# Kernel optimization log

Measured on AMD Instinct MI355X. Metric: run time of the kernel, lower is better.

## Reference

```python
import jax, jax.numpy as jnp
import numpy as np
import math

HIDDEN = 2048
NUM_HEADS = 32
NUM_KV_HEADS = 8
HEAD_DIM = HIDDEN // NUM_HEADS
GROUPS = NUM_HEADS // NUM_KV_HEADS
B, S = 2, 2048


def setup_inputs() -> dict:
    key = jax.random.key(0)
    ks = jax.random.split(key, 9)
    sc = 1.0 / math.sqrt(HIDDEN)
    x = jax.random.normal(ks[0], (B, S, HIDDEN), dtype=jnp.float32)
    # causal mask: 1 where attention allowed, 0 where masked
    mask = jnp.tril(jnp.ones((S, S), dtype=jnp.int32))[None, None, :, :]
    Wq = jax.random.normal(ks[1], (HIDDEN, HIDDEN), dtype=jnp.float32) * sc
    bq = jnp.zeros((HIDDEN,), dtype=jnp.float32)
    Wk = jax.random.normal(ks[2], (NUM_KV_HEADS * HEAD_DIM, HIDDEN), dtype=jnp.float32) * sc
    bk = jnp.zeros((NUM_KV_HEADS * HEAD_DIM,), dtype=jnp.float32)
    Wv = jax.random.normal(ks[3], (NUM_KV_HEADS * HEAD_DIM, HIDDEN), dtype=jnp.float32) * sc
    bv = jnp.zeros((NUM_KV_HEADS * HEAD_DIM,), dtype=jnp.float32)
    Wo = jax.random.normal(ks[4], (HIDDEN, HIDDEN), dtype=jnp.float32) * sc
    bo = jnp.zeros((HIDDEN,), dtype=jnp.float32)
    return {"x": x, "mask": mask, "Wq": Wq, "bq": bq, "Wk": Wk, "bk": bk,
            "Wv": Wv, "bv": bv, "Wo": Wo, "bo": bo}


def reference(x, mask, Wq, bq, Wk, bk, Wv, bv, Wo, bo):
    b, s, _ = x.shape
    # projections (torch Linear: y = x @ W.T + b)
    Q = (x @ Wq.T + bq).reshape(b, s, NUM_HEADS, HEAD_DIM).transpose(0, 2, 1, 3)  # b h s d
    K = (x @ Wk.T + bk).reshape(b, s, NUM_KV_HEADS, HEAD_DIM).transpose(0, 2, 1, 3)
    V = (x @ Wv.T + bv).reshape(b, s, NUM_KV_HEADS, HEAD_DIM).transpose(0, 2, 1, 3)
    # repeat_kv expansion
    K = jnp.repeat(K, GROUPS, axis=1)  # b h s d
    V = jnp.repeat(V, GROUPS, axis=1)
    scores = jnp.einsum('bhqd,bhkd->bhqk', Q, K) / math.sqrt(HEAD_DIM)
    scores = jnp.where(mask == 0, jnp.float32(-jnp.inf), scores)
    w = jax.nn.softmax(scores, axis=-1)
    # dropout is identity in eval mode
    out = jnp.einsum('bhqk,bhkd->bhqd', w, V)
    out = out.transpose(0, 2, 1, 3).reshape(b, s, HIDDEN)
    return out @ Wo.T + bo
```

## Files before the change

kernel.cpp:

```cpp
#include <hip/hip_runtime.h>
#include <hip/hip_bf16.h>
#include <stdint.h>

#define HID   2048
#define SLEN  2048
#define NB    2
#define NHEADS 32
#define NKVH   8
#define HDIM   64
#define KVW    512

typedef __bf16 bf16_t;
typedef __bf16 bf16x2 __attribute__((ext_vector_type(2)));
typedef __bf16 bf16x4 __attribute__((ext_vector_type(4)));
typedef __bf16 bf16x8 __attribute__((ext_vector_type(8)));
typedef float  f32x4  __attribute__((ext_vector_type(4)));

__device__ __forceinline__ f32x4 mfma16(bf16x8 a, bf16x8 b, f32x4 c) {
  return __builtin_amdgcn_mfma_f32_16x16x32_bf16(a, b, c, 0, 0, 0);
}

__device__ __forceinline__ void gl2lds16(const bf16_t* g, bf16_t* l) {
  __builtin_amdgcn_global_load_lds(
      (const __attribute__((address_space(1))) void*)g,
      (__attribute__((address_space(3))) void*)l,
      16, 0, 0);
}

__device__ __forceinline__ float fast_exp2(float x) {
#if __has_builtin(__builtin_amdgcn_exp2f)
  return __builtin_amdgcn_exp2f(x);
#else
  return __expf(x * 0.69314718f);
#endif
}

__device__ __forceinline__ bf16x8 ld8(const bf16_t* p) {
  return *(const bf16x8*)p;
}
__device__ __forceinline__ bf16x8 ld8(const float* p) {
  f32x4 a = *(const f32x4*)p;
  f32x4 b = *(const f32x4*)(p + 4);
  bf16x8 r;
  r[0] = (bf16_t)a[0]; r[1] = (bf16_t)a[1]; r[2] = (bf16_t)a[2]; r[3] = (bf16_t)a[3];
  r[4] = (bf16_t)b[0]; r[5] = (bf16_t)b[1]; r[6] = (bf16_t)b[2]; r[7] = (bf16_t)b[3];
  return r;
}

__device__ __forceinline__ uint32_t pack2(float a, float b) {
  bf16x2 t; t[0] = (bf16_t)a; t[1] = (bf16_t)b;
  return __builtin_bit_cast(uint32_t, t);
}

__device__ __forceinline__ void st_c(bf16_t* p, float v) { *p = (bf16_t)v; }
__device__ __forceinline__ void st_c(float*  p, float v) { *p = v; }

__global__ __launch_bounds__(256) void cvt_kernel(
    const float* __restrict__ x,  const float* __restrict__ wq,
    const float* __restrict__ wk, const float* __restrict__ wv,
    const float* __restrict__ wo,
    const float* __restrict__ bq, const float* __restrict__ bk,
    const float* __restrict__ bv,
    bf16_t* xb, bf16_t* wqb, bf16_t* wkb, bf16_t* wvb, bf16_t* wob,
    float* bcat)
{
  if (blockIdx.y >= 5) {
    const float* fs; float* fd; size_t n;
    if (blockIdx.y == 5)      { fs = bq; fd = bcat;        n = HID; }
    else if (blockIdx.y == 6) { fs = bk; fd = bcat + HID;  n = KVW; }
    else                      { fs = bv; fd = bcat + HID + KVW; n = KVW; }
    const size_t stride4 = (size_t)gridDim.x * 256 * 4;
    for (size_t i = ((size_t)blockIdx.x * 256 + threadIdx.x) * 4; i < n; i += stride4)
      *(f32x4*)(fd + i) = *(const f32x4*)(fs + i);
    return;
  }
  const float* s; bf16_t* d; size_t n;
  switch (blockIdx.y) {
    case 0:  s = x;  d = xb;  n = (size_t)NB * SLEN * HID; break;
    case 1:  s = wq; d = wqb; n = (size_t)HID * HID; break;
    case 2:  s = wk; d = wkb; n = (size_t)KVW * HID; break;
    case 3:  s = wv; d = wvb; n = (size_t)KVW * HID; break;
    default: s = wo; d = wob; n = (size_t)HID * HID; break;
  }
  const size_t stride = (size_t)gridDim.x * 256 * 8;
  for (size_t i = ((size_t)blockIdx.x * 256 + threadIdx.x) * 8; i < n; i += stride)
    *(bf16x8*)(d + i) = ld8(s + i);
}

__device__ __forceinline__ bf16x8 ldfrag(const bf16_t* __restrict__ Lh, int r, int g) {
  return *(const bf16x8*)(Lh + r * 64 + ((g ^ (r & 7)) << 3));
}

template <int Q>
__device__ __forceinline__ void mfma_quad(const bf16x8 (&af)[2][2],
                                          const bf16x8 (&bfr)[4][2],
                                          f32x4 (&acc)[8][4]) {
#pragma unroll
  for (int ks = 0; ks < 2; ++ks)
#pragma unroll
    for (int i = 0; i < 2; ++i)
#pragma unroll
      for (int ni = 0; ni < 4; ++ni)
        acc[2 * Q + i][ni] = mfma16(af[i][ks], bfr[ni][ks], acc[2 * Q + i][ni]);
}

__device__ __forceinline__ void phase_barrier() {
  __builtin_amdgcn_s_barrier();
  asm volatile("" ::: "memory");
}

__device__ __forceinline__ void gemm256_core(
    const bf16_t* __restrict__ Ag,
    const bf16_t* __restrict__ Bg,
    bf16_t* __restrict__ lds, f32x4 (&acc)[8][4])
{
  const int tid  = threadIdx.x;
  const int lane = tid & 63;
  const int w    = tid >> 6;
  const int fr   = lane & 15;
  const int quad = lane >> 4;
  const int wr   = w >> 2;
  const int wc   = w & 3;
  const int rbB  = (wc & 1) * 64;

  bf16_t* A0 = lds;
  bf16_t* B0 = lds + 16384;
  bf16_t* A1 = lds + 32768;
  bf16_t* B1 = lds + 49152;
  const bf16_t* Ar0 = A0 + wr * 8192;
  const bf16_t* Br0 = B0 + (wc >> 1) * 8192;
  const bf16_t* Ar1 = A1 + wr * 8192;
  const bf16_t* Br1 = B1 + (wc >> 1) * 8192;

  const f32x4 z4 = {0.f, 0.f, 0.f, 0.f};
#pragma unroll
  for (int i = 0; i < 8; ++i)
#pragma unroll
    for (int j = 0; j < 4; ++j) acc[i][j] = z4;

  auto STAGE = [&](const bf16_t* __restrict__ Gp, bf16_t* __restrict__ Lh) {
#pragma unroll
    for (int j = 0; j < 2; ++j) {
      const int s = j * 512 + tid;
      const int r = s >> 3;
      const int g = (s & 7) ^ (r & 7);
      gl2lds16(Gp + (size_t)r * HID + g * 8, Lh + s * 8);
    }
  };

  STAGE(Bg,                  B0);
  STAGE(Bg + 128 * HID,      B0 + 8192);
  STAGE(Ag,                  A0);
  STAGE(Ag + 128 * HID,      A0 + 8192);
  STAGE(Bg + 64,             B1);
  STAGE(Bg + 128 * HID + 64, B1 + 8192);
  asm volatile("s_waitcnt vmcnt(4)" ::: "memory");
  phase_barrier();

  bf16x8 bfr[4][2], af[2][2];

#pragma unroll 1
  for (int it = 0; it < 16; ++it) {
    const bool more = (it < 15);
    const size_t k1 = (size_t)(2 * it + 1) * 64;
    const size_t k2 = (size_t)(2 * it + 2) * 64;
    const size_t k3 = (size_t)(2 * it + 3) * 64;

#pragma unroll
    for (int ni = 0; ni < 4; ++ni)
#pragma unroll
      for (int ks = 0; ks < 2; ++ks)
        bfr[ni][ks] = ldfrag(Br0, rbB + ni * 16 + fr, ks * 4 + quad);
#pragma unroll
    for (int i = 0; i < 2; ++i)
#pragma unroll
      for (int ks = 0; ks < 2; ++ks)
        af[i][ks] = ldfrag(Ar0, i * 16 + fr, ks * 4 + quad);
    STAGE(Ag + k1, A1);
    phase_barrier();
    asm volatile("s_waitcnt lgkmcnt(0)" ::: "memory");
    __builtin_amdgcn_s_setprio(1);
    mfma_quad<0>(af, bfr, acc);
    __builtin_amdgcn_s_setprio(0);
    phase_barrier();

#pragma unroll
    for (int i = 0; i < 2; ++i)
#pragma unroll
      for (int ks = 0; ks < 2; ++ks)
        af[i][ks] = ldfrag(Ar0, 32 + i * 16 + fr, ks * 4 + quad);
    STAGE(Ag + 128 * HID + k1, A1 + 8192);
    phase_barrier();
    asm volatile("s_waitcnt lgkmcnt(0)" ::: "memory");
    __builtin_amdgcn_s_setprio(1);
    mfma_quad<1>(af, bfr, acc);
    __builtin_amdgcn_s_setprio(0);
    phase_barrier();

#pragma unroll
    for (int i = 0; i < 2; ++i)
#pragma unroll
      for (int ks = 0; ks < 2; ++ks)
        af[i][ks] = ldfrag(Ar0, 64 + i * 16 + fr, ks * 4 + quad);
    if (more) STAGE(Bg + k2, B0);
    phase_barrier();
    asm volatile("s_waitcnt lgkmcnt(0)" ::: "memory");
    __builtin_amdgcn_s_setprio(1);
    mfma_quad<2>(af, bfr, acc);
    __builtin_amdgcn_s_setprio(0);
    phase_barrier();

#pragma unroll
    for (int i = 0; i < 2; ++i)
#pragma unroll
      for (int ks = 0; ks < 2; ++ks)
        af[i][ks] = ldfrag(Ar0, 96 + i * 16 + fr, ks * 4 + quad);
    if (more) STAGE(Bg + 128 * HID + k2, B0 + 8192);
    phase_barrier();
    asm volatile("s_waitcnt lgkmcnt(0)" ::: "memory");
    __builtin_amdgcn_s_setprio(1);
    mfma_quad<3>(af, bfr, acc);
    __builtin_amdgcn_s_setprio(0);
    if (more) { asm volatile("s_waitcnt vmcnt(4)" ::: "memory"); }
    else      { asm volatile("s_waitcnt vmcnt(0)" ::: "memory"); }
    phase_barrier();

#pragma unroll
    for (int ni = 0; ni < 4; ++ni)
#pragma unroll
      for (int ks = 0; ks < 2; ++ks)
        bfr[ni][ks] = ldfrag(Br1, rbB + ni * 16 + fr, ks * 4 + quad);
#pragma unroll
    for (int i = 0; i < 2; ++i)
#pragma unroll
      for (int ks = 0; ks < 2; ++ks)
        af[i][ks] = ldfrag(Ar1, i * 16 + fr, ks * 4 + quad);
    if (more) STAGE(Ag + k2, A0);
    phase_barrier();
    asm volatile("s_waitcnt lgkmcnt(0)" ::: "memory");
    __builtin_amdgcn_s_setprio(1);
    mfma_quad<0>(af, bfr, acc);
    __builtin_amdgcn_s_setprio(0);
    phase_barrier();

#pragma unroll
    for (int i = 0; i < 2; ++i)
#pragma unroll
      for (int ks = 0; ks < 2; ++ks)
        af[i][ks] = ldfrag(Ar1, 32 + i * 16 + fr, ks * 4 + quad);
    if (more) STAGE(Ag + 128 * HID + k2, A0 + 8192);
    phase_barrier();
    asm volatile("s_waitcnt lgkmcnt(0)" ::: "memory");
    __builtin_amdgcn_s_setprio(1);
    mfma_quad<1>(af, bfr, acc);
    __builtin_amdgcn_s_setprio(0);
    phase_barrier();

#pragma unroll
    for (int i = 0; i < 2; ++i)
#pragma unroll
      for (int ks = 0; ks < 2; ++ks)
        af[i][ks] = ldfrag(Ar1, 64 + i * 16 + fr, ks * 4 + quad);
    if (more) STAGE(Bg + k3, B1);
    phase_barrier();
    asm volatile("s_waitcnt lgkmcnt(0)" ::: "memory");
    __builtin_amdgcn_s_setprio(1);
    mfma_quad<2>(af, bfr, acc);
    __builtin_amdgcn_s_setprio(0);
    phase_barrier();

#pragma unroll
    for (int i = 0; i < 2; ++i)
#pragma unroll
      for (int ks = 0; ks < 2; ++ks)
        af[i][ks] = ldfrag(Ar1, 96 + i * 16 + fr, ks * 4 + quad);
    if (more) STAGE(Bg + 128 * HID + k3, B1 + 8192);
    phase_barrier();
    asm volatile("s_waitcnt lgkmcnt(0)" ::: "memory");
    __builtin_amdgcn_s_setprio(1);
    mfma_quad<3>(af, bfr, acc);
    __builtin_amdgcn_s_setprio(0);
    if (more) { asm volatile("s_waitcnt vmcnt(4)" ::: "memory"); }
    phase_barrier();
  }
}

__global__ __launch_bounds__(512, 2) void qkv8_kernel(
    const bf16_t* __restrict__ xb, const bf16_t* __restrict__ Wcat,
    const float* __restrict__ bcat,
    bf16_t* __restrict__ Qb, bf16_t* __restrict__ Kb, bf16_t* __restrict__ VbT)
{
  __shared__ __align__(16) bf16_t lds[65536];
  const int cb = blockIdx.x;
  const int mb = blockIdx.y;
  f32x4 acc[8][4];
  gemm256_core(xb + (size_t)mb * 256 * HID, Wcat + (size_t)cb * 256 * HID, lds, acc);

  const int tid = threadIdx.x, lane = tid & 63, w = tid >> 6;
  const int fr = lane & 15, quad = lane >> 4, wr = w >> 2, wc = w & 3;
#pragma unroll
  for (int ni = 0; ni < 4; ++ni) {
    const int gcol = cb * 256 + wc * 64 + ni * 16 + fr;
    const float bz = bcat[gcol];
#pragma unroll
    for (int mi = 0; mi < 8; ++mi) {
      const int grow = mb * 256 + wr * 128 + mi * 16 + quad * 4;
      if (cb < 8) {
#pragma unroll
        for (int r = 0; r < 4; ++r)
          Qb[(size_t)(grow + r) * HID + gcol] = (bf16_t)(acc[mi][ni][r] + bz);
      } else if (cb < 10) {
        const int kc = gcol - 2048;
#pragma unroll
        for (int r = 0; r < 4; ++r)
          Kb[(size_t)(grow + r) * KVW + kc] = (bf16_t)(acc[mi][ni][r] + bz);
      } else {
        const int vc = gcol - 2560;
        const int b = grow >> 11, s = grow & 2047;
        bf16x4 pk;
#pragma unroll
        for (int r = 0; r < 4; ++r) pk[r] = (bf16_t)(acc[mi][ni][r] + bz);
        *(bf16x4*)&VbT[((size_t)(b * NKVH + (vc >> 6)) * HDIM + (vc & 63)) * SLEN + s] = pk;
      }
    }
  }
}

__global__ __launch_bounds__(512, 2) void oproj8_kernel(
    const bf16_t* __restrict__ A, const bf16_t* __restrict__ Wob,
    const float* __restrict__ bo, float* __restrict__ out)
{
  __shared__ __align__(16) bf16_t lds[65536];
  const int cb = blockIdx.x;
  const int mb = blockIdx.y;
  f32x4 acc[8][4];
  gemm256_core(A + (size_t)mb * 256 * HID, Wob + (size_t)cb * 256 * HID, lds, acc);

  const int tid = threadIdx.x, lane = tid & 63, w = tid >> 6;
  const int fr = lane & 15, quad = lane >> 4, wr = w >> 2, wc = w & 3;
#pragma unroll
  for (int ni = 0; ni < 4; ++ni) {
    const int gcol = cb * 256 + wc * 64 + ni * 16 + fr;
    const float bz = bo[gcol];
#pragma unroll
    for (int mi = 0; mi < 8; ++mi) {
      const int grow = mb * 256 + wr * 128 + mi * 16 + quad * 4;
#pragma unroll
      for (int r = 0; r < 4; ++r)
        out[(size_t)(grow + r) * HID + gcol] = acc[mi][ni][r] + bz;
    }
  }
}

template <typename AT, typename CT>
__device__ __forceinline__ void gemm128_tile(
    const AT* __restrict__ Ap, int lda,
    const float* __restrict__ Wp, int ldw,
    const float* __restrict__ biasp,
    CT* __restrict__ Cp, int ldc,
    int K)
{
  __shared__ __align__(16) bf16_t Al[128 * 32];
  __shared__ __align__(16) bf16_t Bl[128 * 32];

  const int tid  = threadIdx.x;
  const int lane = tid & 63;
  const int w    = tid >> 6;
  const int fr   = lane & 15;
  const int quad = lane >> 4;
  const int wm   = (w >> 1) * 64;
  const int wn   = (w & 1) * 64;

  const f32x4 z4 = {0.f, 0.f, 0.f, 0.f};
  f32x4 acc[4][4];
  for (int i = 0; i < 4; ++i)
    for (int j = 0; j < 4; ++j) acc[i][j] = z4;

  const int c0    = w * 2;
  const int srow0 = lane >> 2;
  const int skc   = (lane & 3) * 8;

  for (int k0 = 0; k0 < K; k0 += 32) {
    bf16x8 av[2], bv[2];
    for (int t = 0; t < 2; ++t) {
      const int r = (c0 + t) * 16 + srow0;
      av[t] = ld8(Ap + (size_t)r * lda + k0 + skc);
      bv[t] = ld8(Wp + (size_t)r * ldw + k0 + skc);
    }
    for (int t = 0; t < 2; ++t) {
      const int c = c0 + t;
      *(bf16x8*)&Al[c * 512 + lane * 8] = av[t];
      *(bf16x8*)&Bl[c * 512 + lane * 8] = bv[t];
    }
    __syncthreads();
    bf16x8 af[4], bfr[4];
    for (int mi = 0; mi < 4; ++mi)
      af[mi] = *(const bf16x8*)&Al[(wm + mi * 16 + fr) * 32 + quad * 8];
    for (int ni = 0; ni < 4; ++ni)
      bfr[ni] = *(const bf16x8*)&Bl[(wn + ni * 16 + fr) * 32 + quad * 8];
    for (int mi = 0; mi < 4; ++mi)
      for (int ni = 0; ni < 4; ++ni)
        acc[mi][ni] = mfma16(af[mi], bfr[ni], acc[mi][ni]);
    __syncthreads();
  }

  for (int ni = 0; ni < 4; ++ni) {
    const int col = wn + ni * 16 + fr;
    const float bz = biasp[col];
    for (int mi = 0; mi < 4; ++mi) {
      const int r0 = wm + mi * 16 + quad * 4;
      for (int r = 0; r < 4; ++r)
        st_c(Cp + (size_t)(r0 + r) * ldc + col, acc[mi][ni][r] + bz);
    }
  }
}

__global__ __launch_bounds__(256) void qkv_kernel(
    const float* __restrict__ x,
    const float* __restrict__ Wq, const float* __restrict__ bq,
    const float* __restrict__ Wk, const float* __restrict__ bk,
    const float* __restrict__ Wv, const float* __restrict__ bv,
    bf16_t* Qb, bf16_t* Kb, bf16_t* Vb)
{
  const int nb = blockIdx.x;
  const int mb = blockIdx.y;
  const float* W; const float* bias; bf16_t* C; int ldc;
  if (nb < 16)      { W = Wq + (size_t)nb * 128 * HID;  bias = bq + nb * 128;
                      C = Qb + nb * 128; ldc = HID; }
  else if (nb < 20) { const int j = nb - 16;
                      W = Wk + (size_t)j * 128 * HID;   bias = bk + j * 128;
                      C = Kb + j * 128; ldc = KVW; }
  else              { const int j = nb - 20;
                      W = Wv + (size_t)j * 128 * HID;   bias = bv + j * 128;
                      C = Vb + j * 128; ldc = KVW; }
  gemm128_tile<float, bf16_t>(x + (size_t)mb * 128 * HID, HID, W, HID, bias,
                              C + (size_t)mb * 128 * ldc, ldc, HID);
}

__global__ __launch_bounds__(256) void oproj_kernel(
    const bf16_t* __restrict__ A, const float* __restrict__ Wo,
    const float* __restrict__ bo, float* out)
{
  const int nb = blockIdx.x, mb = blockIdx.y;
  gemm128_tile<bf16_t, float>(A + (size_t)mb * 128 * HID, HID,
                              Wo + (size_t)nb * 128 * HID, HID,
                              bo + nb * 128,
                              out + (size_t)mb * 128 * HID + nb * 128, HID, HID);
}

__global__ __launch_bounds__(256) void vtrans_kernel(
    const bf16_t* __restrict__ Vb, bf16_t* __restrict__ VbT)
{
  __shared__ bf16_t T[64][72];
  const int st = blockIdx.x, kvh = blockIdx.y, b = blockIdx.z;
  const int tid = threadIdx.x;
  {
    const int row = tid >> 2;
    const int c16 = (tid & 3) * 16;
    const bf16_t* src =
        Vb + ((size_t)b * SLEN + st * 64 + row) * KVW + kvh * HDIM + c16;
    *(bf16x8*)&T[row][c16]     = *(const bf16x8*)(src);
    *(bf16x8*)&T[row][c16 + 8] = *(const bf16x8*)(src + 8);
  }
  __syncthreads();
  {
    const int d  = tid >> 2;
    const int sc = (tid & 3) * 16;
    bf16_t tmp[16];
    for (int j = 0; j < 16; ++j) tmp[j] = T[sc + j][d];
    bf16_t* dst = VbT + ((size_t)(b * NKVH + kvh) * HDIM + d) * SLEN + st * 64 + sc;
    *(bf16x8*)dst       = *(bf16x8*)&tmp[0];
    *(bf16x8*)(dst + 8) = *(bf16x8*)&tmp[8];
  }
}

__global__ __launch_bounds__(256, 4) void attn_kernel(
    const bf16_t* Q, const bf16_t* __restrict__ Kg,
    const bf16_t* __restrict__ VT, bf16_t* O)
{
  const int pid = blockIdx.x;
  const int h   = blockIdx.y;
  const int b   = blockIdx.z;
  const int kvh = h >> 2;

  const int tid  = threadIdx.x;
  const int lane = tid & 63;
  const int w    = tid >> 6;
  const int fr   = lane & 15;
  const int quad = lane >> 4;

  __shared__ __align__(16) bf16_t KL[8192];
  __shared__ __align__(16) bf16_t VtL[8192];

  const size_t qbase = (size_t)b * SLEN;
  const bf16_t* VTh = VT + (size_t)(b * NKVH + kvh) * HDIM * SLEN;

  const int sigma8 = ((quad & 1) << 4) | ((quad & 2) << 2);
  const bool oddq = (quad & 1);

  bf16x8 ones8;
  {
    const bf16_t o1 = (bf16_t)(fr == 0 ? 1.0f : 0.0f);
#pragma unroll
    for (int j = 0; j < 8; ++j) ones8[j] = o1;
  }

  for (int half = 0; half < 2; ++half) {
    const int qt = half ? (31 - pid) : pid;
    const int q0 = qt * 64;

    bf16x8 qf[2];
#pragma unroll
    for (int ks = 0; ks < 2; ++ks)
      qf[ks] = *(const bf16x8*)&Q[(qbase + q0 + w * 16 + fr) * HID
                                  + h * HDIM + ks * 32 + quad * 8];

    const f32x4 z4 = {0.f, 0.f, 0.f, 0.f};
    f32x4 o_acc[4];
    f32x4 o_l = z4;
#pragma unroll
    for (int di = 0; di < 4; ++di) o_acc[di] = z4;

    const int ktmax = qt >> 1;
    const int qloc  = (qt & 1) * 64 + w * 16 + fr;

    for (int kt = 0; kt <= ktmax; ++kt) {
      const size_t krow0 = qbase + (size_t)kt * 128;

#pragma unroll
      for (int j = 0; j < 4; ++j) {
        const int s  = j * 256 + tid;
        const int ks = s >> 9, kr = (s >> 2) & 127, c8 = s & 3;
        gl2lds16(&Kg[(krow0 + kr) * KVW + kvh * HDIM + ks * 32 + c8 * 8],
                 &KL[s * 8]);
      }
#pragma unroll
      for (int j = 0; j < 4; ++j) {
        const int idx = j * 256 + tid;
        const int kb = idx >> 8, d = (idx >> 2) & 63, c8 = idx & 3;
        gl2lds16(&VTh[(size_t)d * SLEN + kt * 128 + kb * 32 + c8 * 8],
                 &VtL[idx * 8]);
      }
      __syncthreads();

      f32x4 s8[8];
#pragma unroll
      for (int ki = 0; ki < 8; ++ki) s8[ki] = z4;
#pragma unroll
      for (int ks = 0; ks < 2; ++ks)
#pragma unroll
        for (int ki = 0; ki < 8; ++ki) {
          bf16x8 kf = *(const bf16x8*)&KL[ks * 4096 + (ki * 16 + fr) * 32 + quad * 8];
          s8[ki] = mfma16(kf, qf[ks], s8[ki]);
        }

      const float C2 = 0.18033688f;
      const bool diag = (kt == ktmax);

#pragma unroll
      for (int m = 0; m < 4; ++m) {
        float pe[8];
#pragma unroll
        for (int ki2 = 0; ki2 < 2; ++ki2) {
          const int ki = 2 * m + ki2;
#pragma unroll
          for (int r = 0; r < 4; ++r) {
            float p = fast_exp2(s8[ki][r] * C2);
            if (diag && (ki * 16 + quad * 4 + r > qloc)) p = 0.f;
            pe[ki2 * 4 + r] = p;
          }
        }
        uint32_t pw0 = pack2(pe[0], pe[1]);
        uint32_t pw1 = pack2(pe[2], pe[3]);
        uint32_t pw2 = pack2(pe[4], pe[5]);
        uint32_t pw3 = pack2(pe[6], pe[7]);
        uint32_t x0 = oddq ? pw0 : pw2;
        uint32_t x1 = oddq ? pw1 : pw3;
        uint32_t r0 = (uint32_t)__shfl_xor((int)x0, 16);
        uint32_t r1 = (uint32_t)__shfl_xor((int)x1, 16);
        union { uint32_t u[4]; bf16x8 v; } pb;
        pb.u[0] = oddq ? r0 : pw0;
        pb.u[1] = oddq ? r1 : pw1;
        pb.u[2] = oddq ? pw2 : r0;
        pb.u[3] = oddq ? pw3 : r1;

        o_l = mfma16(pb.v, ones8, o_l);
#pragma unroll
        for (int di = 0; di < 4; ++di) {
          bf16x8 vf = *(const bf16x8*)&VtL[m * 2048 + (di * 16 + fr) * 32 + sigma8];
          o_acc[di] = mfma16(pb.v, vf, o_acc[di]);
        }
      }
      __syncthreads();
    }

#pragma unroll
    for (int r = 0; r < 4; ++r) {
      const float l  = __shfl(o_l[r], lane & 48);
      const float rl = 1.f / l;
      const size_t qg = qbase + q0 + w * 16 + quad * 4 + r;
#pragma unroll
      for (int di = 0; di < 4; ++di)
        O[qg * HID + h * HDIM + di * 16 + fr] = (bf16_t)(o_acc[di][r] * rl);
    }
  }
}

extern "C" void kernel_launch(void* const* d_in, const int* in_sizes, int n_in,
                              void* d_out, int out_size, void* d_ws, size_t ws_size,
                              hipStream_t stream) {
  const float* x  = (const float*)d_in[0];
  const float* Wq = (const float*)d_in[2];
  const float* bq = (const float*)d_in[3];
  const float* Wk = (const float*)d_in[4];
  const float* bk = (const float*)d_in[5];
  const float* Wv = (const float*)d_in[6];
  const float* bv = (const float*)d_in[7];
  const float* Wo = (const float*)d_in[8];
  const float* bo = (const float*)d_in[9];
  float* out = (float*)d_out;

  const size_t M = (size_t)NB * SLEN;
  dim3 blk(256, 1, 1);

  const size_t needA = (M * HID
                        + (size_t)HID * HID
                        + (size_t)KVW * HID
                        + (size_t)KVW * HID
                        + (size_t)HID * HID
                        + M * HID
                        + M * KVW
                        + M * KVW) * 2
                       + (size_t)(HID + 2 * KVW) * sizeof(float);
  if (ws_size >= needA) {
    bf16_t* xb  = (bf16_t*)d_ws;
    bf16_t* Wqb = xb  + M * HID;
    bf16_t* Wkb = Wqb + (size_t)HID * HID;
    bf16_t* Wvb = Wkb + (size_t)KVW * HID;
    bf16_t* Wob = Wvb + (size_t)KVW * HID;
    bf16_t* Qb  = Wob + (size_t)HID * HID;
    bf16_t* Kb  = Qb  + M * HID;
    bf16_t* VbT = Kb  + M * KVW;
    float*  bcat = (float*)(VbT + M * KVW);

    cvt_kernel<<<dim3(1024, 8, 1), blk, 0, stream>>>(
        x, Wq, Wk, Wv, Wo, bq, bk, bv, xb, Wqb, Wkb, Wvb, Wob, bcat);
    qkv8_kernel<<<dim3(12, 16, 1), dim3(512, 1, 1), 0, stream>>>(
        xb, Wqb, bcat, Qb, Kb, VbT);
    attn_kernel<<<dim3(16, 32, 2), blk, 0, stream>>>(Qb, Kb, VbT, Qb);
    oproj8_kernel<<<dim3(8, 16, 1), dim3(512, 1, 1), 0, stream>>>(
        Qb, Wob, bo, out);
  } else {
    bf16_t* Qb  = (bf16_t*)d_ws;
    bf16_t* Kb  = Qb + M * HID;
    bf16_t* Vb  = Kb + M * KVW;
    bf16_t* VbT = Vb + M * KVW;

    qkv_kernel<<<dim3(24, 32, 1), blk, 0, stream>>>(x, Wq, bq, Wk, bk, Wv, bv, Qb, Kb, Vb);
    vtrans_kernel<<<dim3(32, 8, 2), blk, 0, stream>>>(Vb, VbT);
    attn_kernel<<<dim3(16, 32, 2), blk, 0, stream>>>(Qb, Kb, VbT, Qb);
    oproj_kernel<<<dim3(16, 32, 1), blk, 0, stream>>>(Qb, Wo, bo, out);
  }
}
```

Measured before the change: 315.7 us.

## Swizzle K/V shared-memory layout and remap attention blocks to XCDs by KV head

The attention kernel now stores K and V^T tiles in LDS with an XOR swizzle on the 16-byte column chunk, keyed on row bits, and reads them back with the matching swizzle. The aim is to avoid LDS bank conflicts on the fragment reads. The launch becomes a flat 1024-block grid whose block index is decoded so that all blocks sharing a KV head land on the same XCD, which should improve L2 reuse of K/V. The change depends on round-robin block-to-XCD dispatch, and the swizzle must stay consistent between the writes and the reads.

```diff
diff --git a/kernel.cpp b/kernel.cpp
--- a/kernel.cpp
+++ b/kernel.cpp
@@ -478,10 +478,14 @@
     const bf16_t* Q, const bf16_t* __restrict__ Kg,
     const bf16_t* __restrict__ VT, bf16_t* O)
 {
-  const int pid = blockIdx.x;
-  const int h   = blockIdx.y;
-  const int b   = blockIdx.z;
-  const int kvh = h >> 2;
+  const int bid = blockIdx.x;
+  const int xcd = bid & 7;
+  const int j   = bid >> 3;
+  const int kvh = xcd;
+  const int b   = j >> 6;
+  const int rem = j & 63;
+  const int h   = kvh * 4 + (rem & 3);
+  const int pid = rem >> 2;
 
   const int tid  = threadIdx.x;
   const int lane = tid & 63;
@@ -495,14 +499,15 @@
   const size_t qbase = (size_t)b * SLEN;
   const bf16_t* VTh = VT + (size_t)(b * NKVH + kvh) * HDIM * SLEN;
 
-  const int sigma8 = ((quad & 1) << 4) | ((quad & 2) << 2);
+  const int sig = ((quad & 1) << 1) | ((quad >> 1) & 1);
+  const int fsw = (fr >> 1) & 3;
   const bool oddq = (quad & 1);
 
   bf16x8 ones8;
   {
     const bf16_t o1 = (bf16_t)(fr == 0 ? 1.0f : 0.0f);
 #pragma unroll
-    for (int j = 0; j < 8; ++j) ones8[j] = o1;
+    for (int j2 = 0; j2 < 8; ++j2) ones8[j2] = o1;
   }
 
   for (int half = 0; half < 2; ++half) {
@@ -528,16 +533,16 @@
       const size_t krow0 = qbase + (size_t)kt * 128;
 
 #pragma unroll
-      for (int j = 0; j < 4; ++j) {
-        const int s  = j * 256 + tid;
-        const int ks = s >> 9, kr = (s >> 2) & 127, c8 = s & 3;
+      for (int jj = 0; jj < 4; ++jj) {
+        const int s  = jj * 256 + tid;
+        const int ks = s >> 9, kr = (s >> 2) & 127, c8 = (s & 3) ^ ((kr >> 1) & 3);
         gl2lds16(&Kg[(krow0 + kr) * KVW + kvh * HDIM + ks * 32 + c8 * 8],
                  &KL[s * 8]);
       }
 #pragma unroll
-      for (int j = 0; j < 4; ++j) {
-        const int idx = j * 256 + tid;
-        const int kb = idx >> 8, d = (idx >> 2) & 63, c8 = idx & 3;
+      for (int jj = 0; jj < 4; ++jj) {
+        const int idx = jj * 256 + tid;
+        const int kb = idx >> 8, d = (idx >> 2) & 63, c8 = (idx & 3) ^ ((d >> 1) & 3);
         gl2lds16(&VTh[(size_t)d * SLEN + kt * 128 + kb * 32 + c8 * 8],
                  &VtL[idx * 8]);
       }
@@ -550,7 +555,8 @@
       for (int ks = 0; ks < 2; ++ks)
 #pragma unroll
         for (int ki = 0; ki < 8; ++ki) {
-          bf16x8 kf = *(const bf16x8*)&KL[ks * 4096 + (ki * 16 + fr) * 32 + quad * 8];
+          bf16x8 kf = *(const bf16x8*)&KL[ks * 4096 + (ki * 16 + fr) * 32
+                                          + ((quad ^ fsw) << 3)];
           s8[ki] = mfma16(kf, qf[ks], s8[ki]);
         }
 
@@ -587,7 +593,8 @@
         o_l = mfma16(pb.v, ones8, o_l);
 #pragma unroll
         for (int di = 0; di < 4; ++di) {
-          bf16x8 vf = *(const bf16x8*)&VtL[m * 2048 + (di * 16 + fr) * 32 + sigma8];
+          bf16x8 vf = *(const bf16x8*)&VtL[m * 2048 + (di * 16 + fr) * 32
+                                           + ((sig ^ fsw) << 3)];
           o_acc[di] = mfma16(pb.v, vf, o_acc[di]);
         }
       }
@@ -647,18 +654,18 @@
         x, Wq, Wk, Wv, Wo, bq, bk, bv, xb, Wqb, Wkb, Wvb, Wob, bcat);
     qkv8_kernel<<<dim3(12, 16, 1), dim3(512, 1, 1), 0, stream>>>(
         xb, Wqb, bcat, Qb, Kb, VbT);
-    attn_kernel<<<dim3(16, 32, 2), blk, 0, stream>>>(Qb, Kb, VbT, Qb);
+    attn_kernel<<<dim3(1024, 1, 1), blk, 0, stream>>>(Qb, Kb, VbT, Qb);
     oproj8_kernel<<<dim3(8, 16, 1), dim3(512, 1, 1), 0, stream>>>(
         Qb, Wob, bo, out);
   } else {
     bf16_t* Qb  = (bf16_t*)d_ws;
-    bf16_t* Kb  = Qb + M * HID;
+    bf16_t* Kb  = Qb + M * KVW * 0 + M * HID;
     bf16_t* Vb  = Kb + M * KVW;
     bf16_t* VbT = Vb + M * KVW;
 
     qkv_kernel<<<dim3(24, 32, 1), blk, 0, stream>>>(x, Wq, bq, Wk, bk, Wv, bv, Qb, Kb, Vb);
     vtrans_kernel<<<dim3(32, 8, 2), blk, 0, stream>>>(Vb, VbT);
-    attn_kernel<<<dim3(16, 32, 2), blk, 0, stream>>>(Qb, Kb, VbT, Qb);
+    attn_kernel<<<dim3(1024, 1, 1), blk, 0, stream>>>(Qb, Kb, VbT, Qb);
     oproj_kernel<<<dim3(16, 32, 1), blk, 0, stream>>>(Qb, Wo, bo, out);
   }
 }
```

New measurement: 320.6 us. Within noise of the previous version (+1.5%).
